# Performance work log

Measured on AMD Instinct MI355X. Metric: run time of the kernel, lower is better.

## Reference

```python
import jax, jax.numpy as jnp
import numpy as np

EPS_GN = 1e-8
EPS_ATTN = 1e-8


def setup_inputs() -> dict:
    key = jax.random.key(0)
    ks = jax.random.split(key, 13)
    B, C, N = 4, 512, 2048
    s = 0.02
    return {
        "x": jax.random.normal(ks[0], (B, C, N), jnp.float32),
        "dw_w": jax.random.normal(ks[1], (C, 3), jnp.float32) * s,
        "pw_w": jax.random.normal(ks[2], (C, C), jnp.float32) * s,
        "u_w": jax.random.normal(ks[3], (2 * C, C), jnp.float32) * s,
        "u_b": jax.random.normal(ks[4], (2 * C,), jnp.float32) * s,
        "v_w": jax.random.normal(ks[5], (2 * C, C), jnp.float32) * s,
        "v_b": jax.random.normal(ks[6], (2 * C,), jnp.float32) * s,
        "h_w": jax.random.normal(ks[7], (C, C), jnp.float32) * s,
        "h_b": jax.random.normal(ks[8], (C,), jnp.float32) * s,
        "q_w": jax.random.normal(ks[9], (C, C), jnp.float32) * s,
        "k_w": jax.random.normal(ks[10], (C, C), jnp.float32) * s,
        "o_w": jax.random.normal(ks[11], (C, 2 * C), jnp.float32) * s,
        "o_b": jax.random.normal(ks[12], (C,), jnp.float32) * s,
    }


def reference(x, dw_w, pw_w, u_w, u_b, v_w, v_b, h_w, h_b, q_w, k_w, o_w, o_b):
    # x: [B, C, N]
    C = x.shape[1]
    # GroupNorm(1, C): normalize over (C, N) per sample; affine is identity-init
    # in torch but we follow the module math with default weight=1, bias=0
    mean = jnp.mean(x, axis=(1, 2), keepdims=True)
    var = jnp.var(x, axis=(1, 2), keepdims=True)
    z = (x - mean) * jax.lax.rsqrt(var + EPS_GN)

    # local depthwise conv k=3, pad=1 (cross-correlation), no bias
    zp = jnp.pad(z, ((0, 0), (0, 0), (1, 1)))
    dw = (dw_w[:, 0, None] * zp[:, :, :-2]
          + dw_w[:, 1, None] * zp[:, :, 1:-1]
          + dw_w[:, 2, None] * zp[:, :, 2:])
    # pointwise conv (no bias)
    z = z + jnp.einsum('oc,bcn->bon', pw_w, dw)

    u = jax.nn.sigmoid(jnp.einsum('oc,bcn->bon', u_w, z) + u_b[:, None])  # [B,2C,N]
    v = jnp.einsum('oc,bcn->bon', v_w, z) + v_b[:, None]                  # [B,2C,N]
    h = jnp.einsum('oc,bcn->bno', h_w, z) + h_b                           # [B,N,C]

    q = h @ q_w.T  # [B,N,C]
    k = h @ k_w.T  # [B,N,C]
    scale = 1.0 / jnp.sqrt(jnp.float32(C))

    logits = jnp.einsum('bnc,bmc->bnm', q, k) * scale
    a = jax.nn.relu(logits)
    a = a * a
    a = a / (jnp.sum(a, axis=-1, keepdims=True) + EPS_ATTN)

    av = jnp.einsum('bnm,bom->bon', a, v)  # [B,2C,N]
    y = jnp.einsum('oc,bcn->bon', o_w, u * av) + o_b[:, None]
    return x + y
```

## Files before the change

### kernel.cpp

```cpp
#include <hip/hip_runtime.h>
#include <hip/hip_bf16.h>
#include <cstdint>

typedef __bf16 bhalf;
typedef __bf16 bhalf8 __attribute__((ext_vector_type(8)));
typedef float f32x4 __attribute__((ext_vector_type(4)));

enum { EPI_Z2=0, EPI_UV=1, EPI_BIAS=2, EPI_QK=3, EPI_ATTN=4, EPI_PV=5, EPI_Y=6 };

__device__ __forceinline__ void gl_lds16(const bhalf* g, bhalf* l) {
  __builtin_amdgcn_global_load_lds(
      (const __attribute__((address_space(1))) unsigned int*)g,
      (__attribute__((address_space(3))) unsigned int*)l,
      16, 0, 0);
}
__device__ __forceinline__ void barrier_raw() { asm volatile("s_barrier" ::: "memory"); }
#define VMW(n)  asm volatile("s_waitcnt vmcnt(" #n ")" ::: "memory")
#define LGKM0() asm volatile("s_waitcnt lgkmcnt(0)" ::: "memory")


template<int EPI>
__global__ void __launch_bounds__(512, 2)
gA(const bhalf* __restrict__ A, const bhalf* __restrict__ Bw,
   void* __restrict__ Out, void* __restrict__ Out2,
   const float* __restrict__ bias, const float* __restrict__ bias2,
   int N, int K, long sA, long sB, long sO, long sAuxf, float scale)
{
  constexpr int KSL = 256*64;
  constexpr int REG = 2*KSL;
  constexpr int DBUF = 2*REG;
  __shared__ __align__(16) char lds[2*DBUF];

  const int gx = gridDim.x, gy = gridDim.y;
  const int nwg = gx*gy;
  const int flat = blockIdx.y*gx + blockIdx.x;
  const int q8 = nwg>>3, r8 = nwg&7, xcd = flat&7, o8 = flat>>3;
  const int wsw = (xcd<r8 ? xcd*(q8+1) : r8*(q8+1)+(xcd-r8)*q8) + o8;
  const int bx = wsw % gx, by = wsw / gx;
  const int m0 = by*256, n0 = bx*256;
  const int bz = blockIdx.z;

  const bhalf* Ab = A + (long)bz*sA;
  const bhalf* Bb = Bw + (long)bz*sB;

  const int tid = threadIdx.x, wid = tid>>6, lane = tid&63;
  const int lm = lane&15, kq = lane>>4;
  const int wm = wid>>2, wn = wid&3;
  const int srow = lane>>2;
  const int csw = ((lane&3) ^ ((lane>>3)&3)) * 8;
  const int kqs = kq ^ ((lm>>1)&3);

  f32x4 acc[8][4];
  #pragma unroll
  for (int i=0;i<8;i++)
    #pragma unroll
    for (int j=0;j<4;j++) acc[i][j] = f32x4{0.f,0.f,0.f,0.f};

  auto stageA = [&](int kt){
    char* base = lds + (kt&1)*DBUF;
    const int k0 = kt*64;
    #pragma unroll
    for (int h=0; h<2; h++)
      #pragma unroll
      for (int ksl=0; ksl<2; ksl++){
        bhalf* d = (bhalf*)(base + ksl*KSL + (h*128 + wid*16)*64);
        gl_lds16(Ab + (long)(m0 + h*128 + wid*16 + srow)*K + k0 + ksl*32 + csw, d);
      }
  };
  auto stageB = [&](int kt){
    char* base = lds + (kt&1)*DBUF + REG;
    const int k0 = kt*64;
    #pragma unroll
    for (int h=0; h<2; h++)
      #pragma unroll
      for (int ksl=0; ksl<2; ksl++){
        bhalf* d = (bhalf*)(base + ksl*KSL + (h*128 + wid*16)*64);
        gl_lds16(Bb + (long)(n0 + h*128 + wid*16 + srow)*K + k0 + ksl*32 + csw, d);
      }
  };

  bhalf8 af[4][2], bf[4][2];
  auto readA = [&](int kt, int ih){
    char* base = lds + (kt&1)*DBUF;
    #pragma unroll
    for (int i2=0;i2<4;i2++)
      #pragma unroll
      for (int ksl=0;ksl<2;ksl++)
        af[i2][ksl] = *(const bhalf8*)(base + ksl*KSL + (wm*128 + ih*64 + i2*16 + lm)*64 + kqs*16);
  };
  auto readB = [&](int kt, int jh){
    char* base = lds + (kt&1)*DBUF + REG;
    #pragma unroll
    for (int j2=0;j2<2;j2++)
      #pragma unroll
      for (int ksl=0;ksl<2;ksl++)
        bf[jh*2+j2][ksl] = *(const bhalf8*)(base + ksl*KSL + (wn*64 + jh*32 + j2*16 + lm)*64 + kqs*16);
  };
  auto mfma16 = [&](int ih, int jh){
    __builtin_amdgcn_s_setprio(1);
    #pragma unroll
    for (int i2=0;i2<4;i2++)
      #pragma unroll
      for (int j2=0;j2<2;j2++)
        #pragma unroll
        for (int ksl=0;ksl<2;ksl++)
          acc[ih*4+i2][jh*2+j2] = __builtin_amdgcn_mfma_f32_16x16x32_bf16(
              af[i2][ksl], bf[jh*2+j2][ksl], acc[ih*4+i2][jh*2+j2], 0,0,0);
    __builtin_amdgcn_s_setprio(0);
  };

  const int NT = K>>6;
  stageA(0); stageB(0); stageA(1);
  for (int kt=0; kt<NT; ++kt){
    if (kt==NT-1) { VMW(0); } else { VMW(4); }
    barrier_raw();
    readA(kt,0); readB(kt,0);
    if (kt+1<NT) stageB(kt+1);
    mfma16(0,0);
    barrier_raw();
    readB(kt,1);
    mfma16(0,1);
    barrier_raw();
    readA(kt,1);
    mfma16(1,0);
    barrier_raw();
    if (kt+2<NT) stageA(kt+2);
    mfma16(1,1);
  }
  barrier_raw();

  if constexpr (EPI==EPI_ATTN){
    float rs[8][4];
    #pragma unroll
    for (int i=0;i<8;i++)
      #pragma unroll
      for (int r=0;r<4;r++) rs[i][r]=0.f;
    #pragma unroll
    for (int i=0;i<8;i++){
      #pragma unroll
      for (int j=0;j<4;j++){
        const int lcol = wn*64 + j*16 + lm;
        #pragma unroll
        for (int r=0;r<4;r++){
          const int lrow = wm*128 + i*16 + kq*4 + r;
          float v = acc[i][j][r];
          v *= scale; v = fmaxf(v,0.f); v = v*v;
          rs[i][r] += v;
          const int cb = lcol*2;
          const int lb = lrow*512 + (((cb>>5) ^ ((lrow>>2)&3))<<5) + (cb&31);
          *(bhalf*)(lds + lb) = (bhalf)v;
        }
      }
    }
    float* rd = (float*)Out2;
    #pragma unroll
    for (int i=0;i<8;i++){
      const int rbase = m0 + wm*128 + i*16 + kq*4;
      #pragma unroll
      for (int r=0;r<4;r++){
        float s = rs[i][r];
        s += __shfl_xor(s,1); s += __shfl_xor(s,2);
        s += __shfl_xor(s,4); s += __shfl_xor(s,8);
        if (lm==0) atomicAdd(rd + (long)bz*sAuxf + rbase + r, s);
      }
    }
    LGKM0();
    barrier_raw();
    char* obase = (char*)Out + 2*((long)bz*sO + (long)m0*N + n0);
    const int ldb = N*2;
    #pragma unroll
    for (int it=0; it<16; ++it){
      const int g = (it*512 + tid)*16;
      const int row = g >> 9, off = g & 511;
      const int lb = row*512 + (((off>>5) ^ ((row>>2)&3))<<5) + (off&31);
      uint4 val = *(const uint4*)(lds + lb);
      *(uint4*)(obase + (long)row*ldb + off) = val;
    }
  }
  if constexpr (EPI==EPI_UV){
    const bool uh = n0 < 1024;
    const float* bv = uh ? bias : bias2;
    const int bc0 = uh ? n0 : n0-1024;
    #pragma unroll
    for (int i=0;i<8;i++){
      #pragma unroll
      for (int j=0;j<4;j++){
        const int lcol = wn*64 + j*16 + lm;
        #pragma unroll
        for (int r=0;r<4;r++){
          const int lrow = wm*128 + i*16 + kq*4 + r;
          float v = acc[i][j][r] + bv[bc0 + lcol];
          if (uh){
            v = 1.f/(1.f + __expf(-v));
            const int cb = lcol*2;
            const int lb = lrow*512 + (((cb>>5) ^ ((lrow>>2)&3))<<5) + (cb&31);
            *(bhalf*)(lds + lb) = (bhalf)v;
          } else {
            const int lb = lcol*512 + 2*(lrow ^ ((lcol&15)<<2));
            *(bhalf*)(lds + lb) = (bhalf)v;
          }
        }
      }
    }
    LGKM0();
    barrier_raw();
    if (uh){
      char* obase = (char*)Out + 2*((long)m0*1024 + n0);
      #pragma unroll
      for (int it=0; it<16; ++it){
        const int g = (it*512 + tid)*16;
        const int row = g >> 9, off = g & 511;
        const int lb = row*512 + (((off>>5) ^ ((row>>2)&3))<<5) + (off&31);
        uint4 val = *(const uint4*)(lds + lb);
        *(uint4*)(obase + (long)row*2048 + off) = val;
      }
    } else {
      char* vb = (char*)Out2 + 2*((long)(m0>>11)*1024*2048 + (long)(n0-1024)*2048 + (m0 & 2047));
      #pragma unroll
      for (int it=0; it<16; ++it){
        const int g = (it*512 + tid)*16;
        const int row = g >> 9, off = g & 511;
        const int t0 = off >> 1;
        const int s = (row&15)<<2;
        unsigned long long lo = *(const unsigned long long*)(lds + row*512 + 2*(t0^s));
        unsigned long long hi = *(const unsigned long long*)(lds + row*512 + 2*((t0+4)^s));
        char* dst = vb + (long)row*4096 + off;
        ((unsigned long long*)dst)[0] = lo;
        ((unsigned long long*)dst)[1] = hi;
      }
    }
  }
  (void)scale; (void)bias; (void)bias2; (void)N;
}

template<int EPI>
__global__ void __launch_bounds__(256, 2)
gw(const bhalf* __restrict__ A, const bhalf* __restrict__ Bw,
   void* __restrict__ Out, void* __restrict__ Out2,
   const bhalf* __restrict__ auxb, const float* __restrict__ auxf,
   int N, int K, long sB, float scale, int rowshift)
{
  constexpr int DBUF = 384*64;
  __shared__ __align__(16) char lds[3*DBUF];

  const int gx = gridDim.x, gy = gridDim.y;
  const int nwg = gx*gy;
  const int flat = blockIdx.y*gx + blockIdx.x;
  const int q8 = nwg>>3, r8 = nwg&7, xcd = flat&7, o8 = flat>>3;
  const int wsw = (xcd<r8 ? xcd*(q8+1) : r8*(q8+1)+(xcd-r8)*q8) + o8;
  const int bx = wsw % gx, by = wsw / gx;
  const int m0 = by*256, n0 = bx*128;

  const bhalf* Ab = A;
  const bhalf* Bb = Bw + (rowshift ? (long)(m0>>rowshift)*sB : 0);

  const int tid = threadIdx.x, wid = tid>>6, lane = tid&63;
  const int lm = lane&15, kq = lane>>4;
  const int wm = wid>>1, wn = wid&1;
  const int srow = lane>>2;
  const int csw = ((lane&3) ^ ((lane>>3)&3)) * 8;
  const int kqs = kq ^ ((lm>>1)&3);

  f32x4 acc[8][4];
  #pragma unroll
  for (int i=0;i<8;i++)
    #pragma unroll
    for (int j=0;j<4;j++) acc[i][j] = f32x4{0.f,0.f,0.f,0.f};

  auto stage = [&](int kt){
    char* base = lds + (kt%3)*DBUF;
    const int k0 = kt*32;
    #pragma unroll
    for (int c=0;c<6;c++){
      const int r0 = wid*96 + c*16;
      bhalf* d = (bhalf*)(base + r0*64);
      const bhalf* g = (r0 < 256)
        ? Ab + (long)(m0 + r0 + srow)*K + k0 + csw
        : Bb + (long)(n0 + r0 - 256 + srow)*K + k0 + csw;
      gl_lds16(g, d);
    }
  };

  bhalf8 af[8], bf[4];
  auto readA = [&](int kt){
    char* base = lds + (kt%3)*DBUF;
    #pragma unroll
    for (int i=0;i<8;i++)
      af[i] = *(const bhalf8*)(base + (wm*128 + i*16 + lm)*64 + kqs*16);
  };
  auto readB = [&](int kt, int jh){
    char* base = lds + (kt%3)*DBUF;
    #pragma unroll
    for (int j2=0;j2<2;j2++)
      bf[jh*2+j2] = *(const bhalf8*)(base + (256 + wn*64 + jh*32 + j2*16 + lm)*64 + kqs*16);
  };
  auto mfma16 = [&](int jh){
    __builtin_amdgcn_s_setprio(1);
    #pragma unroll
    for (int i=0;i<8;i++)
      #pragma unroll
      for (int j2=0;j2<2;j2++)
        acc[i][jh*2+j2] = __builtin_amdgcn_mfma_f32_16x16x32_bf16(
            af[i], bf[jh*2+j2], acc[i][jh*2+j2], 0,0,0);
    __builtin_amdgcn_s_setprio(0);
  };

  const int NT = K>>5;
  stage(0); stage(1);
  for (int kt=0; kt<NT; ++kt){
    if (kt==NT-1) { VMW(0); } else { VMW(6); }
    barrier_raw();
    readA(kt); readB(kt,0);
    if (kt+2<NT) stage(kt+2);
    mfma16(0);
    barrier_raw();
    readB(kt,1);
    mfma16(1);
  }
  barrier_raw();

  char* obase; int ldb;
  if constexpr (EPI==EPI_PV){
    obase = (char*)Out + 2*((long)m0*1024 + n0); ldb = 2048;
  }
  if constexpr (EPI==EPI_QK){
    bool qh = n0 < 512;
    obase = (char*)(qh?Out:Out2) + 2*((long)m0*512 + (n0 - (qh?0:512)));
    ldb = 1024;
  }
  #pragma unroll
  for (int i=0;i<8;i++){
    #pragma unroll
    for (int j=0;j<4;j++){
      const int lcol = wn*64 + j*16 + lm;
      #pragma unroll
      for (int r=0;r<4;r++){
        const int lrow = wm*128 + i*16 + kq*4 + r;
        float v = acc[i][j][r];
        if constexpr (EPI==EPI_PV){
          const int rowg = m0 + lrow;
          float den = auxf[rowg];
          v *= __builtin_amdgcn_rcpf(den + 1e-8f);
          v *= (float)auxb[(long)rowg*1024 + n0 + lcol];
        }
        const int cb = lcol*2;
        const int lb = lrow*256 + (((cb>>5) ^ ((lrow>>2)&3))<<5) + (cb&31);
        *(bhalf*)(lds + lb) = (bhalf)v;
      }
    }
  }
  LGKM0();
  barrier_raw();
  #pragma unroll
  for (int it=0; it<16; ++it){
    const int g = (it*256 + tid)*16;
    const int row = g >> 8, off = g & 255;
    const int lb = row*256 + (((off>>5) ^ ((row>>2)&3))<<5) + (off&31);
    uint4 val = *(const uint4*)(lds + lb);
    *(uint4*)(obase + (long)row*ldb + off) = val;
  }
  (void)scale; (void)auxb; (void)auxf; (void)N;
}

template<int EPI>
__global__ void __launch_bounds__(256, 2)
g4k(const bhalf* __restrict__ A, const bhalf* __restrict__ Bw,
    void* __restrict__ Out,
    const float* __restrict__ bias,
    const bhalf* __restrict__ auxb,
    const float* __restrict__ xadd,
    int M, int N, int K)
{
  constexpr int KSL = 256*64;
  constexpr int DBUF = 2*KSL;
  __shared__ __align__(16) char lds[2*DBUF];

  const int gx = gridDim.x, gy = gridDim.y;
  const int nwg = gx*gy;
  const int flat = blockIdx.y*gx + blockIdx.x;
  const int q8 = nwg>>3, r8 = nwg&7, xcd = flat&7, o8 = flat>>3;
  const int w = (xcd<r8 ? xcd*(q8+1) : r8*(q8+1)+(xcd-r8)*q8) + o8;
  const int bx = w % gx, by = w / gx;
  const int m0 = by*128, n0 = bx*128;

  const int tid = threadIdx.x;
  const int wid = tid>>6, lane = tid&63;
  const int lm = lane&15, kq = lane>>4;
  const int wm = wid>>1, wn = wid&1;
  const int srow = lane>>2;
  const int csw = ((lane&3) ^ ((lane>>3)&3))*8;
  const int kqs = kq ^ ((lm>>1)&3);

  f32x4 acc[4][4];
  #pragma unroll
  for (int i=0;i<4;i++)
    #pragma unroll
    for (int j=0;j<4;j++) acc[i][j] = f32x4{0.f,0.f,0.f,0.f};

  auto stage = [&](int kt){
    char* base = lds + (kt&1)*DBUF;
    const int k0 = kt*64;
    #pragma unroll
    for (int c=0;c<4;c++){
      const int r0 = c*64 + wid*16;
      #pragma unroll
      for (int ksl=0; ksl<2; ksl++){
        bhalf* d = (bhalf*)(base + ksl*KSL + r0*64);
        const bhalf* g = (r0 < 128)
          ? A  + (long)(m0 + r0 + srow)*K + k0 + ksl*32 + csw
          : Bw + (long)(n0 + r0 - 128 + srow)*K + k0 + ksl*32 + csw;
        gl_lds16(g, d);
      }
    }
  };

  bhalf8 af[4][2], bf[4][2];
  auto readA = [&](int kt){
    char* base = lds + (kt&1)*DBUF;
    #pragma unroll
    for (int i2=0;i2<4;i2++)
      #pragma unroll
      for (int ksl=0;ksl<2;ksl++)
        af[i2][ksl] = *(const bhalf8*)(base + ksl*KSL + (wm*64 + i2*16 + lm)*64 + kqs*16);
  };
  auto readB = [&](int kt, int jh){
    char* base = lds + (kt&1)*DBUF;
    #pragma unroll
    for (int j2=0;j2<2;j2++)
      #pragma unroll
      for (int ksl=0;ksl<2;ksl++)
        bf[jh*2+j2][ksl] = *(const bhalf8*)(base + ksl*KSL + (128 + wn*64 + jh*32 + j2*16 + lm)*64 + kqs*16);
  };
  auto mfma16 = [&](int jh){
    __builtin_amdgcn_s_setprio(1);
    #pragma unroll
    for (int i2=0;i2<4;i2++)
      #pragma unroll
      for (int j2=0;j2<2;j2++)
        #pragma unroll
        for (int ksl=0;ksl<2;ksl++)
          acc[i2][jh*2+j2] = __builtin_amdgcn_mfma_f32_16x16x32_bf16(
              af[i2][ksl], bf[jh*2+j2][ksl], acc[i2][jh*2+j2], 0,0,0);
    __builtin_amdgcn_s_setprio(0);
  };

  const int NT = K>>6;
  stage(0); stage(1);
  for (int kt=0; kt<NT; ++kt){
    if (kt==NT-1) { VMW(0); } else { VMW(8); }
    barrier_raw();
    readA(kt); readB(kt,0);
    mfma16(0);
    barrier_raw();
    readB(kt,1);
    if (kt+2<NT) stage(kt+2);
    mfma16(1);
  }
  barrier_raw();

  if constexpr (EPI==EPI_Y){
    #pragma unroll
    for (int i=0;i<4;i++){
      #pragma unroll
      for (int j=0;j<4;j++){
        const int lcol = wn*64 + j*16 + lm;
        #pragma unroll
        for (int r=0;r<4;r++){
          const int lrow = wm*64 + i*16 + kq*4 + r;
          float v = acc[i][j][r] + bias[n0 + lcol];
          const int lb = lcol*512 + 4*(lrow ^ ((lcol&15)<<2));
          *(float*)(lds + lb) = v;
        }
      }
    }
    LGKM0();
    barrier_raw();
    const int b = m0 >> 11, nb = m0 & 2047;
    float* ob = (float*)Out + ((long)b*512 + n0)*2048 + nb;
    const float* xb = xadd + ((long)b*512 + n0)*2048 + nb;
    #pragma unroll
    for (int it=0; it<16; ++it){
      const int g = (it*256 + tid)*16;
      const int row = g >> 9, off = g & 511;
      const int t0 = off >> 2;
      const int s = (row&15)<<2;
      f32x4 vv = *(const f32x4*)(lds + row*512 + 4*(t0^s));
      f32x4 xx = *(const f32x4*)(xb + (long)row*2048 + t0);
      *(f32x4*)(ob + (long)row*2048 + t0) = vv + xx;
    }
  } else {
    char* obase = (char*)Out + 2*((long)m0*N + n0);
    const int ldb = N*2;
    #pragma unroll
    for (int i=0;i<4;i++){
      #pragma unroll
      for (int j=0;j<4;j++){
        const int lcol = wn*64 + j*16 + lm;
        #pragma unroll
        for (int r=0;r<4;r++){
          const int lrow = wm*64 + i*16 + kq*4 + r;
          float v = acc[i][j][r];
          if constexpr (EPI==EPI_Z2)
            v += (float)auxb[(long)(m0+lrow)*N + n0 + lcol];
          if constexpr (EPI==EPI_BIAS)
            v += bias[n0 + lcol];
          const int cb = lcol*2;
          const int lb = lrow*256 + (((cb>>5) ^ ((lrow>>2)&3))<<5) + (cb&31);
          *(bhalf*)(lds + lb) = (bhalf)v;
        }
      }
    }
    LGKM0();
    barrier_raw();
    #pragma unroll
    for (int it=0; it<8; ++it){
      const int g = (it*256 + tid)*16;
      const int row = g >> 8, off = g & 255;
      const int lb = row*256 + (((off>>5) ^ ((row>>2)&3))<<5) + (off&31);
      uint4 val = *(const uint4*)(lds + lb);
      *(uint4*)(obase + (long)row*ldb + off) = val;
    }
  }
  (void)M; (void)xadd; (void)bias; (void)auxb;
}

struct CvtArgs { const float* src[7]; bhalf* dst[7]; int n[7]; };
__global__ void cvt_multi(CvtArgs a) {
  int seg = blockIdx.y;
  int i = (blockIdx.x*256 + threadIdx.x)*4;
  if (i >= a.n[seg]) return;
  float4 f = *(const float4*)(a.src[seg] + i);
  bhalf* d = a.dst[seg] + i;
  d[0]=(bhalf)f.x; d[1]=(bhalf)f.y; d[2]=(bhalf)f.z; d[3]=(bhalf)f.w;
}

__global__ void gn_part(const float* __restrict__ x, float* __restrict__ ps, float* __restrict__ pss) {
  int b = blockIdx.y;
  const float* xb = x + (long)b*(512*2048);
  float s=0.f, ss=0.f;
  #pragma unroll
  for (int it=0; it<8; it++){
    int idx = ((it*128 + blockIdx.x)*256 + threadIdx.x)*4;
    float4 f = *(const float4*)(xb + idx);
    s  += f.x+f.y+f.z+f.w;
    ss += f.x*f.x+f.y*f.y+f.z*f.z+f.w*f.w;
  }
  for (int off=32; off; off>>=1){ s += __shfl_xor(s,off); ss += __shfl_xor(ss,off); }
  __shared__ float ls[4], lss[4];
  int wid = threadIdx.x>>6, lane = threadIdx.x&63;
  if (lane==0){ ls[wid]=s; lss[wid]=ss; }
  __syncthreads();
  if (threadIdx.x==0){
    s = ls[0]+ls[1]+ls[2]+ls[3]; ss = lss[0]+lss[1]+lss[2]+lss[3];
    ps[b*128 + blockIdx.x] = s; pss[b*128 + blockIdx.x] = ss;
  }
}

__global__ void gn_final(const float* __restrict__ ps, const float* __restrict__ pss,
                         float* __restrict__ stats) {
  int b = blockIdx.x;
  float s = ps[b*128 + threadIdx.x], ss = pss[b*128 + threadIdx.x];
  for (int off=32; off; off>>=1){ s += __shfl_xor(s,off); ss += __shfl_xor(ss,off); }
  __shared__ float l0[2], l1[2];
  int wid = threadIdx.x>>6, lane = threadIdx.x&63;
  if (lane==0){ l0[wid]=s; l1[wid]=ss; }
  __syncthreads();
  if (threadIdx.x==0){
    s = l0[0]+l0[1]; ss = l1[0]+l1[1];
    float mean = s*(1.f/1048576.f);
    float var  = ss*(1.f/1048576.f) - mean*mean;
    stats[b*2] = mean; stats[b*2+1] = rsqrtf(var + 1e-8f);
  }
}

__global__ void norm_dw_T(const float* __restrict__ x, const float* __restrict__ stats,
                          const float* __restrict__ dw_w,
                          bhalf* __restrict__ zT, bhalf* __restrict__ dwT) {
  int b = blockIdx.z, n0 = blockIdx.x*32, c0 = blockIdx.y*32;
  float mean = stats[b*2], rstd = stats[b*2+1];
  __shared__ float zs[32][35];
  int tx = threadIdx.x, ty = threadIdx.y;
  #pragma unroll
  for (int r=0;r<4;r++){
    int c = c0 + ty + r*8;
    for (int cc=tx; cc<34; cc+=32){
      int n = n0 - 1 + cc;
      float v = 0.f;
      if (n>=0 && n<2048) v = (x[((long)b*512 + c)*2048 + n] - mean)*rstd;
      zs[ty + r*8][cc] = v;
    }
  }
  __syncthreads();
  float w0 = dw_w[(c0+tx)*3+0], w1 = dw_w[(c0+tx)*3+1], w2 = dw_w[(c0+tx)*3+2];
  #pragma unroll
  for (int r=0;r<4;r++){
    int ln = ty + r*8;
    float z = zs[tx][ln+1];
    float d = w0*zs[tx][ln] + w1*zs[tx][ln+1] + w2*zs[tx][ln+2];
    long o = ((long)b*2048 + n0 + ln)*512 + c0 + tx;
    zT[o] = (bhalf)z; dwT[o] = (bhalf)d;
  }
}

extern "C" void kernel_launch(void* const* d_in, const int* in_sizes, int n_in,
                              void* d_out, int out_size, void* d_ws, size_t ws_size,
                              hipStream_t stream) {
  (void)in_sizes; (void)n_in; (void)out_size; (void)ws_size;
  const float* x    = (const float*)d_in[0];
  const float* dw_w = (const float*)d_in[1];
  const float* pw_w = (const float*)d_in[2];
  const float* u_w  = (const float*)d_in[3];
  const float* u_b  = (const float*)d_in[4];
  const float* v_w  = (const float*)d_in[5];
  const float* v_b  = (const float*)d_in[6];
  const float* h_w  = (const float*)d_in[7];
  const float* h_b  = (const float*)d_in[8];
  const float* q_w  = (const float*)d_in[9];
  const float* k_w  = (const float*)d_in[10];
  const float* o_w  = (const float*)d_in[11];
  const float* o_b  = (const float*)d_in[12];
  float* out = (float*)d_out;

  char* ws = (char*)d_ws;
  size_t off = 0;
  auto alloc = [&](size_t bytes) -> void* {
    void* p = ws + off; off = (off + bytes + 255) & ~(size_t)255; return p;
  };

  float* ps    = (float*)alloc(4*128*4);
  float* pss   = (float*)alloc(4*128*4);
  float* stats = (float*)alloc(4*2*4);
  float* rden  = (float*)alloc(4*2048*4);
  bhalf* wb_pw = (bhalf*)alloc(512*512*2);
  bhalf* wb_uv = (bhalf*)alloc((size_t)2048*512*2);
  bhalf* wb_h  = (bhalf*)alloc(512*512*2);
  bhalf* wb_qk = (bhalf*)alloc((size_t)1024*512*2);
  bhalf* wb_o  = (bhalf*)alloc((size_t)512*1024*2);
  const size_t ACT = (size_t)4*2048*512;
  bhalf* zT   = (bhalf*)alloc(ACT*2);
  bhalf* dwT  = (bhalf*)alloc(ACT*2);
  bhalf* z2T  = (bhalf*)alloc(ACT*2);
  bhalf* ub   = (bhalf*)alloc(ACT*2*2);
  bhalf* v_fm = (bhalf*)alloc(ACT*2*2);
  bhalf* hb   = (bhalf*)alloc(ACT*2);
  bhalf* wsc  = (bhalf*)alloc((size_t)4*2048*2048*2);
  bhalf* uav  = (bhalf*)alloc(ACT*2*2);
  bhalf* qb = zT;  bhalf* kb = dwT;

  hipMemsetAsync(rden, 0, 4*2048*4, stream);

  CvtArgs ca;
  ca.src[0]=pw_w; ca.dst[0]=wb_pw;           ca.n[0]=512*512;
  ca.src[1]=u_w;  ca.dst[1]=wb_uv;           ca.n[1]=1024*512;
  ca.src[2]=v_w;  ca.dst[2]=wb_uv+1024*512;  ca.n[2]=1024*512;
  ca.src[3]=h_w;  ca.dst[3]=wb_h;            ca.n[3]=512*512;
  ca.src[4]=q_w;  ca.dst[4]=wb_qk;           ca.n[4]=512*512;
  ca.src[5]=k_w;  ca.dst[5]=wb_qk+512*512;   ca.n[5]=512*512;
  ca.src[6]=o_w;  ca.dst[6]=wb_o;            ca.n[6]=512*1024;
  cvt_multi<<<dim3(512,7), 256, 0, stream>>>(ca);

  gn_part<<<dim3(128,4), 256, 0, stream>>>(x, ps, pss);
  gn_final<<<dim3(4), 128, 0, stream>>>(ps, pss, stats);

  norm_dw_T<<<dim3(64,16,4), dim3(32,8), 0, stream>>>(x, stats, dw_w, zT, dwT);

  const float iscl = 0.044194173824159216f;
  g4k<EPI_Z2><<<dim3(4,64,1), 256, 0, stream>>>(dwT, wb_pw, z2T,
      nullptr, zT, nullptr, 8192, 512, 512);
  gA<EPI_UV><<<dim3(8,32,1), 512, 0, stream>>>(z2T, wb_uv, ub, v_fm,
      u_b, v_b, 2048, 512, 0, 0, 0, 0, 0.f);
  g4k<EPI_BIAS><<<dim3(4,64,1), 256, 0, stream>>>(z2T, wb_h, hb,
      h_b, nullptr, nullptr, 8192, 512, 512);
  gw<EPI_QK><<<dim3(8,32,1), 256, 0, stream>>>(hb, wb_qk, qb, kb,
      nullptr, nullptr, 1024, 512, 0, 0.f, 0);
  gA<EPI_ATTN><<<dim3(8,8,4), 512, 0, stream>>>(qb, kb, wsc, rden,
      nullptr, nullptr, 2048, 512,
      (long)2048*512, (long)2048*512, (long)2048*2048, 2048, iscl);
  gw<EPI_PV><<<dim3(8,32,1), 256, 0, stream>>>(wsc, v_fm, uav, nullptr,
      ub, rden, 1024, 2048, (long)1024*2048, 0.f, 11);
  g4k<EPI_Y><<<dim3(4,64,1), 256, 0, stream>>>(uav, wb_o, out,
      o_b, nullptr, x, 8192, 512, 1024);
}
```

Measured before the change: 191.2 us.

## Replace 256x128 gw kernel with 128x128 g4k for QK and PV GEMMs

Removes the separate gw kernel (256x128 tile, K-step 32, triple-buffered) and routes the QK projection and PV GEMMs through the g4k kernel, which uses a 128x128 tile with K-step 64 and double buffering. g4k gains per-block B offset (rowshift), dual output, and the PV epilogue (divide by denominator, multiply by u). Grids double from 256 to 512 blocks, which should improve occupancy and wave balance across CUs. The cost is less per-block operand reuse and more global traffic per FLOP.

```diff
diff --git a/kernel.cpp b/kernel.cpp
--- a/kernel.cpp
+++ b/kernel.cpp
@@ -235,141 +235,12 @@
 
 template<int EPI>
 __global__ void __launch_bounds__(256, 2)
-gw(const bhalf* __restrict__ A, const bhalf* __restrict__ Bw,
-   void* __restrict__ Out, void* __restrict__ Out2,
-   const bhalf* __restrict__ auxb, const float* __restrict__ auxf,
-   int N, int K, long sB, float scale, int rowshift)
-{
-  constexpr int DBUF = 384*64;
-  __shared__ __align__(16) char lds[3*DBUF];
-
-  const int gx = gridDim.x, gy = gridDim.y;
-  const int nwg = gx*gy;
-  const int flat = blockIdx.y*gx + blockIdx.x;
-  const int q8 = nwg>>3, r8 = nwg&7, xcd = flat&7, o8 = flat>>3;
-  const int wsw = (xcd<r8 ? xcd*(q8+1) : r8*(q8+1)+(xcd-r8)*q8) + o8;
-  const int bx = wsw % gx, by = wsw / gx;
-  const int m0 = by*256, n0 = bx*128;
-
-  const bhalf* Ab = A;
-  const bhalf* Bb = Bw + (rowshift ? (long)(m0>>rowshift)*sB : 0);
-
-  const int tid = threadIdx.x, wid = tid>>6, lane = tid&63;
-  const int lm = lane&15, kq = lane>>4;
-  const int wm = wid>>1, wn = wid&1;
-  const int srow = lane>>2;
-  const int csw = ((lane&3) ^ ((lane>>3)&3)) * 8;
-  const int kqs = kq ^ ((lm>>1)&3);
-
-  f32x4 acc[8][4];
-  #pragma unroll
-  for (int i=0;i<8;i++)
-    #pragma unroll
-    for (int j=0;j<4;j++) acc[i][j] = f32x4{0.f,0.f,0.f,0.f};
-
-  auto stage = [&](int kt){
-    char* base = lds + (kt%3)*DBUF;
-    const int k0 = kt*32;
-    #pragma unroll
-    for (int c=0;c<6;c++){
-      const int r0 = wid*96 + c*16;
-      bhalf* d = (bhalf*)(base + r0*64);
-      const bhalf* g = (r0 < 256)
-        ? Ab + (long)(m0 + r0 + srow)*K + k0 + csw
-        : Bb + (long)(n0 + r0 - 256 + srow)*K + k0 + csw;
-      gl_lds16(g, d);
-    }
-  };
-
-  bhalf8 af[8], bf[4];
-  auto readA = [&](int kt){
-    char* base = lds + (kt%3)*DBUF;
-    #pragma unroll
-    for (int i=0;i<8;i++)
-      af[i] = *(const bhalf8*)(base + (wm*128 + i*16 + lm)*64 + kqs*16);
-  };
-  auto readB = [&](int kt, int jh){
-    char* base = lds + (kt%3)*DBUF;
-    #pragma unroll
-    for (int j2=0;j2<2;j2++)
-      bf[jh*2+j2] = *(const bhalf8*)(base + (256 + wn*64 + jh*32 + j2*16 + lm)*64 + kqs*16);
-  };
-  auto mfma16 = [&](int jh){
-    __builtin_amdgcn_s_setprio(1);
-    #pragma unroll
-    for (int i=0;i<8;i++)
-      #pragma unroll
-      for (int j2=0;j2<2;j2++)
-        acc[i][jh*2+j2] = __builtin_amdgcn_mfma_f32_16x16x32_bf16(
-            af[i], bf[jh*2+j2], acc[i][jh*2+j2], 0,0,0);
-    __builtin_amdgcn_s_setprio(0);
-  };
-
-  const int NT = K>>5;
-  stage(0); stage(1);
-  for (int kt=0; kt<NT; ++kt){
-    if (kt==NT-1) { VMW(0); } else { VMW(6); }
-    barrier_raw();
-    readA(kt); readB(kt,0);
-    if (kt+2<NT) stage(kt+2);
-    mfma16(0);
-    barrier_raw();
-    readB(kt,1);
-    mfma16(1);
-  }
-  barrier_raw();
-
-  char* obase; int ldb;
-  if constexpr (EPI==EPI_PV){
-    obase = (char*)Out + 2*((long)m0*1024 + n0); ldb = 2048;
-  }
-  if constexpr (EPI==EPI_QK){
-    bool qh = n0 < 512;
-    obase = (char*)(qh?Out:Out2) + 2*((long)m0*512 + (n0 - (qh?0:512)));
-    ldb = 1024;
-  }
-  #pragma unroll
-  for (int i=0;i<8;i++){
-    #pragma unroll
-    for (int j=0;j<4;j++){
-      const int lcol = wn*64 + j*16 + lm;
-      #pragma unroll
-      for (int r=0;r<4;r++){
-        const int lrow = wm*128 + i*16 + kq*4 + r;
-        float v = acc[i][j][r];
-        if constexpr (EPI==EPI_PV){
-          const int rowg = m0 + lrow;
-          float den = auxf[rowg];
-          v *= __builtin_amdgcn_rcpf(den + 1e-8f);
-          v *= (float)auxb[(long)rowg*1024 + n0 + lcol];
-        }
-        const int cb = lcol*2;
-        const int lb = lrow*256 + (((cb>>5) ^ ((lrow>>2)&3))<<5) + (cb&31);
-        *(bhalf*)(lds + lb) = (bhalf)v;
-      }
-    }
-  }
-  LGKM0();
-  barrier_raw();
-  #pragma unroll
-  for (int it=0; it<16; ++it){
-    const int g = (it*256 + tid)*16;
-    const int row = g >> 8, off = g & 255;
-    const int lb = row*256 + (((off>>5) ^ ((row>>2)&3))<<5) + (off&31);
-    uint4 val = *(const uint4*)(lds + lb);
-    *(uint4*)(obase + (long)row*ldb + off) = val;
-  }
-  (void)scale; (void)auxb; (void)auxf; (void)N;
-}
-
-template<int EPI>
-__global__ void __launch_bounds__(256, 2)
 g4k(const bhalf* __restrict__ A, const bhalf* __restrict__ Bw,
-    void* __restrict__ Out,
+    void* __restrict__ Out, void* __restrict__ Out2,
     const float* __restrict__ bias,
-    const bhalf* __restrict__ auxb,
+    const bhalf* __restrict__ auxb, const float* __restrict__ auxf,
     const float* __restrict__ xadd,
-    int M, int N, int K)
+    int M, int N, int K, long sB, int rowshift)
 {
   constexpr int KSL = 256*64;
   constexpr int DBUF = 2*KSL;
@@ -383,6 +254,8 @@
   const int bx = w % gx, by = w / gx;
   const int m0 = by*128, n0 = bx*128;
 
+  const bhalf* Bb = Bw + (rowshift ? (long)(m0>>rowshift)*sB : 0);
+
   const int tid = threadIdx.x;
   const int wid = tid>>6, lane = tid&63;
   const int lm = lane&15, kq = lane>>4;
@@ -408,7 +281,7 @@
         bhalf* d = (bhalf*)(base + ksl*KSL + r0*64);
         const bhalf* g = (r0 < 128)
           ? A  + (long)(m0 + r0 + srow)*K + k0 + ksl*32 + csw
-          : Bw + (long)(n0 + r0 - 128 + srow)*K + k0 + ksl*32 + csw;
+          : Bb + (long)(n0 + r0 - 128 + srow)*K + k0 + ksl*32 + csw;
         gl_lds16(g, d);
       }
     }
@@ -489,8 +362,15 @@
       *(f32x4*)(ob + (long)row*2048 + t0) = vv + xx;
     }
   } else {
-    char* obase = (char*)Out + 2*((long)m0*N + n0);
-    const int ldb = N*2;
+    char* obase; int ldb;
+    if constexpr (EPI==EPI_QK){
+      bool qh = n0 < 512;
+      obase = (char*)(qh?Out:Out2) + 2*((long)m0*512 + (n0 - (qh?0:512)));
+      ldb = 1024;
+    } else {
+      obase = (char*)Out + 2*((long)m0*N + n0);
+      ldb = N*2;
+    }
     #pragma unroll
     for (int i=0;i<4;i++){
       #pragma unroll
@@ -504,6 +384,12 @@
             v += (float)auxb[(long)(m0+lrow)*N + n0 + lcol];
           if constexpr (EPI==EPI_BIAS)
             v += bias[n0 + lcol];
+          if constexpr (EPI==EPI_PV){
+            const int rowg = m0 + lrow;
+            float den = auxf[rowg];
+            v *= __builtin_amdgcn_rcpf(den + 1e-8f);
+            v *= (float)auxb[(long)rowg*1024 + n0 + lcol];
+          }
           const int cb = lcol*2;
           const int lb = lrow*256 + (((cb>>5) ^ ((lrow>>2)&3))<<5) + (cb&31);
           *(bhalf*)(lds + lb) = (bhalf)v;
@@ -521,7 +407,7 @@
       *(uint4*)(obase + (long)row*ldb + off) = val;
     }
   }
-  (void)M; (void)xadd; (void)bias; (void)auxb;
+  (void)M; (void)xadd; (void)bias; (void)auxb; (void)auxf;
 }
 
 struct CvtArgs { const float* src[7]; bhalf* dst[7]; int n[7]; };
@@ -665,19 +551,19 @@
   norm_dw_T<<<dim3(64,16,4), dim3(32,8), 0, stream>>>(x, stats, dw_w, zT, dwT);
 
   const float iscl = 0.044194173824159216f;
-  g4k<EPI_Z2><<<dim3(4,64,1), 256, 0, stream>>>(dwT, wb_pw, z2T,
-      nullptr, zT, nullptr, 8192, 512, 512);
+  g4k<EPI_Z2><<<dim3(4,64,1), 256, 0, stream>>>(dwT, wb_pw, z2T, nullptr,
+      nullptr, zT, nullptr, nullptr, 8192, 512, 512, 0, 0);
   gA<EPI_UV><<<dim3(8,32,1), 512, 0, stream>>>(z2T, wb_uv, ub, v_fm,
       u_b, v_b, 2048, 512, 0, 0, 0, 0, 0.f);
-  g4k<EPI_BIAS><<<dim3(4,64,1), 256, 0, stream>>>(z2T, wb_h, hb,
-      h_b, nullptr, nullptr, 8192, 512, 512);
-  gw<EPI_QK><<<dim3(8,32,1), 256, 0, stream>>>(hb, wb_qk, qb, kb,
-      nullptr, nullptr, 1024, 512, 0, 0.f, 0);
+  g4k<EPI_BIAS><<<dim3(4,64,1), 256, 0, stream>>>(z2T, wb_h, hb, nullptr,
+      h_b, nullptr, nullptr, nullptr, 8192, 512, 512, 0, 0);
+  g4k<EPI_QK><<<dim3(8,64,1), 256, 0, stream>>>(hb, wb_qk, qb, kb,
+      nullptr, nullptr, nullptr, nullptr, 8192, 1024, 512, 0, 0);
   gA<EPI_ATTN><<<dim3(8,8,4), 512, 0, stream>>>(qb, kb, wsc, rden,
       nullptr, nullptr, 2048, 512,
       (long)2048*512, (long)2048*512, (long)2048*2048, 2048, iscl);
-  gw<EPI_PV><<<dim3(8,32,1), 256, 0, stream>>>(wsc, v_fm, uav, nullptr,
-      ub, rden, 1024, 2048, (long)1024*2048, 0.f, 11);
-  g4k<EPI_Y><<<dim3(4,64,1), 256, 0, stream>>>(uav, wb_o, out,
-      o_b, nullptr, x, 8192, 512, 1024);
-}
+  g4k<EPI_PV><<<dim3(8,64,1), 256, 0, stream>>>(wsc, v_fm, uav, nullptr,
+      nullptr, ub, rden, nullptr, 8192, 1024, 2048, (long)1024*2048, 11);
+  g4k<EPI_Y><<<dim3(4,64,1), 256, 0, stream>>>(uav, wb_o, out, nullptr,
+      o_b, nullptr, nullptr, x, 8192, 512, 1024, 0, 0);
+}
```

Result: faster. 183.4 us (-4.1%).
